# Kernel tuning notes

Measured on AMD Instinct MI355X. Metric: run time of the kernel, lower is better.

## Reference

```python
import jax, jax.numpy as jnp
import numpy as np

WEIGHT_FACTOR = 1.0
N_CLUSTERS = 64


def setup_inputs() -> dict:
    key = jax.random.key(0)
    k1, k2, k3 = jax.random.split(key, 3)
    B, H, W = 128, 256, 256
    x = jax.random.uniform(k1, (B, H, W), dtype=jnp.float32)
    pattern_importance = jax.random.uniform(k2, (B, N_CLUSTERS), dtype=jnp.float32)
    # dense cluster map: value in [0, N_CLUSTERS) = cluster id; == N_CLUSTERS = unassigned (mask stays 1)
    cluster_id = jax.random.randint(k3, (H, W), 0, N_CLUSTERS + 1, dtype=jnp.int32)
    return {"x": x, "pattern_importance": pattern_importance, "cluster_id": cluster_id}


def reference(x, pattern_importance, cluster_id):
    # FFT2 over last two dims; torch fftshift with dim=None shifts ALL axes (incl. batch),
    # and jnp.fft.fftshift has the same default semantics.
    x_fft = jnp.fft.fftshift(jnp.fft.fft2(x))
    assigned = cluster_id < N_CLUSTERS                     # [H, W] bool
    cid = jnp.where(assigned, cluster_id, 0)               # safe gather index
    vals = pattern_importance[:, cid] * WEIGHT_FACTOR      # [B, H, W] gather-built mask values
    mask = jnp.where(assigned[None, :, :], vals, jnp.float32(1.0))
    x_reject = x_fft * mask
    x_ifft = jnp.abs(jnp.fft.ifft2(jnp.fft.ifftshift(x_reject)))
    x_diff = jnp.abs(x_ifft - x)
    x_new = jnp.stack([x, x_ifft, x_diff], axis=1)         # [B, 3, H, W]
    return (x_new, pattern_importance)
```

## Files before the change

### kernel.cpp

```cpp
#include <hip/hip_runtime.h>
#include <hip/hip_fp16.h>
#include <math.h>

#define BB 128
#define HH 256
#define WW 256
#define HW 65536
#define OUT_B_STRIDE 196608

typedef float f32x4_t __attribute__((ext_vector_type(4)));

__device__ __forceinline__ void nt_store4(const float4 v, float4* p){
  f32x4_t t;
  t[0] = v.x; t[1] = v.y; t[2] = v.z; t[3] = v.w;
  __builtin_nontemporal_store(t, reinterpret_cast<f32x4_t*>(p));
}

__device__ __forceinline__ float2 cadd(float2 a, float2 b){ return make_float2(a.x+b.x, a.y+b.y); }
__device__ __forceinline__ float2 csub(float2 a, float2 b){ return make_float2(a.x-b.x, a.y-b.y); }

template<bool INV>
__device__ __forceinline__ float2 cmul_t(float2 a, float2 b){
  if (INV) return make_float2(a.x*b.x + a.y*b.y, a.y*b.x - a.x*b.y);
  return make_float2(a.x*b.x - a.y*b.y, a.x*b.y + a.y*b.x);
}

template<bool INV>
__device__ __forceinline__ void fft4(float2&a,float2&b,float2&c,float2&d){
  float2 t0 = cadd(a,c), t1 = csub(a,c);
  float2 t2 = cadd(b,d), t3 = csub(b,d);
  float2 t3r = INV ? make_float2(-t3.y, t3.x) : make_float2(t3.y, -t3.x);
  a = cadd(t0,t2);
  b = cadd(t1,t3r);
  c = csub(t0,t2);
  d = csub(t1,t3r);
}

template<bool INV>
__device__ __forceinline__ void fft16(float2 x[16]){
  #pragma unroll
  for (int j0=0;j0<4;++j0) fft4<INV>(x[j0], x[j0+4], x[j0+8], x[j0+12]);
  const float WR[10] = {1.f, 0.923879533f, 0.707106781f, 0.382683432f, 0.f,
                        0.f, -0.707106781f, 0.f, 0.f, -0.923879533f};
  const float WI[10] = {0.f, -0.382683432f, -0.707106781f, -0.923879533f, -1.f,
                        0.f, -0.707106781f, 0.f, 0.f, 0.382683432f};
  #pragma unroll
  for (int q0=1;q0<4;++q0)
    #pragma unroll
    for (int j0=1;j0<4;++j0){
      int k = j0*q0;
      x[j0+4*q0] = cmul_t<INV>(x[j0+4*q0], make_float2(WR[k], WI[k]));
    }
  #pragma unroll
  for (int q0=0;q0<4;++q0) fft4<INV>(x[4*q0], x[4*q0+1], x[4*q0+2], x[4*q0+3]);
  float2 t[16];
  #pragma unroll
  for (int q0=0;q0<4;++q0)
    #pragma unroll
    for (int q1=0;q1<4;++q1) t[q0+4*q1] = x[4*q0+q1];
  #pragma unroll
  for (int i=0;i<16;++i) x[i]=t[i];
}

__device__ __forceinline__ void build_tw256(float2* tw, int tid){
  float s,c;
  __sincosf(-6.28318530717958647692f * (float)tid / 256.0f, &s, &c);
  tw[tid] = make_float2(c, s);
}

__device__ __forceinline__ uint pkh2(float2 v){
  __half2 h = __float22half2_rn(v);
  return *(uint*)&h;
}
__device__ __forceinline__ float2 uph2(uint u){
  __half2 h = *(__half2*)&u;
  return __half22float2(h);
}

union SharedU {
  float  xs[16*272];
  float2 zbuf[16*273];
  float  ybuf[16*272];
};

__global__ __launch_bounds__(256, 4) void k_row_fwd(const float* __restrict__ x,
                                                    __half2* __restrict__ S,
                                                    const int* __restrict__ cid,
                                                    unsigned char* __restrict__ cidp){
  __shared__ SharedU sh;
  __shared__ float2 tw[256];
  int tid = threadIdx.x;
  int t = tid & 15, r = tid >> 4;
  build_tw256(tw, tid);

  if (blockIdx.x < 64){
    int g = (blockIdx.x*256 + tid) * 4;
    int p  = g >> 8;
    int s  = (g >> 4) & 15;
    int k1b = g & 15;
    int wfreq = 16*(p & 15) + (p >> 4);
    int w2 = (wfreq + 128) & 255;
    uchar4 v4;
    unsigned char* vp = (unsigned char*)&v4;
    #pragma unroll
    for (int i=0;i<4;++i){
      int h2 = (16*(k1b+i) + s + 128) & 255;
      int cv = cid[h2*256 + w2];
      vp[i] = (unsigned char)cv;
    }
    *(uchar4*)(cidp + g) = v4;
  }

  const float4* xb = (const float4*)x + (size_t)blockIdx.x * 1024;
  #pragma unroll
  for (int k=0;k<4;++k){
    int i2 = tid + k*256;
    float4 v = xb[i2];
    int row = i2 >> 6, c4 = i2 & 63;
    *(float4*)&sh.xs[row*272 + c4*4] = v;
  }
  __syncthreads();
  float2 X[16];
  #pragma unroll
  for (int j=0;j<16;++j) X[j] = make_float2(sh.xs[r*272 + 16*j + t], 0.f);
  __syncthreads();
  fft16<false>(X);
  #pragma unroll
  for (int q=0;q<16;++q) X[q] = cmul_t<false>(X[q], tw[t*q]);
  #pragma unroll
  for (int q=0;q<16;++q) sh.zbuf[r*273 + q*17 + t] = X[q];
  __syncthreads();
  float2 Y[16];
  #pragma unroll
  for (int tt=0;tt<16;++tt) Y[tt] = sh.zbuf[r*273 + t*17 + tt];
  fft16<false>(Y);
  int row = blockIdx.x*16 + r;
  int b = row >> 8, h = row & 255;
  uint4* dst = (uint4*)(S + (size_t)b*HW + h*256 + t*16);
  #pragma unroll
  for (int k=0;k<4;++k){
    uint4 q;
    q.x = pkh2(Y[4*k+0]); q.y = pkh2(Y[4*k+1]);
    q.z = pkh2(Y[4*k+2]); q.w = pkh2(Y[4*k+3]);
    dst[k] = q;
  }
}

__global__ __launch_bounds__(256, 4) void k_col(__half2* __restrict__ S,
                                                const unsigned char* __restrict__ cidp,
                                                const float* __restrict__ pi){
  __shared__ SharedU sh;
  __shared__ float2 tw[256];
  __shared__ float sPI[64];
  int tid = threadIdx.x;
  int c = tid & 15, t = tid >> 4;
  int cg = blockIdx.x, b = blockIdx.y;
  build_tw256(tw, tid);
  if (tid < 64) sPI[tid] = pi[(((b + 64) & 127) << 6) + tid] * 0.25f;
  __half2* Sb = S + (size_t)b*HW;
  int p = cg*16 + c;
  float2 X[16];
  #pragma unroll
  for (int j=0;j<16;++j) X[j] = uph2(*(uint*)&Sb[(16*j + t)*256 + p]);
  uint4 mq = *(const uint4*)(cidp + p*256 + t*16);
  __syncthreads();
  fft16<false>(X);
  #pragma unroll
  for (int q=0;q<16;++q) X[q] = cmul_t<false>(X[q], tw[t*q]);
  #pragma unroll
  for (int q=0;q<16;++q) sh.zbuf[c*273 + q*17 + t] = X[q];
  __syncthreads();
  int s = t;
  float2 Y[16];
  #pragma unroll
  for (int tt=0;tt<16;++tt) Y[tt] = sh.zbuf[c*273 + s*17 + tt];
  fft16<false>(Y);
  const uint* mw = (const uint*)&mq;
  #pragma unroll
  for (int k1=0;k1<16;++k1){
    int cv = (mw[k1>>2] >> ((k1&3)*8)) & 255;
    float m = (cv < 64) ? sPI[cv] : 0.25f;
    Y[k1].x *= m; Y[k1].y *= m;
  }
  __syncthreads();
  fft16<true>(Y);
  #pragma unroll
  for (int u=0;u<16;++u) Y[u] = cmul_t<true>(Y[u], tw[u*s]);
  #pragma unroll
  for (int u=0;u<16;++u) sh.zbuf[c*273 + u*17 + s] = Y[u];
  __syncthreads();
  float2 R[16];
  #pragma unroll
  for (int k0=0;k0<16;++k0) R[k0] = sh.zbuf[c*273 + t*17 + k0];
  fft16<true>(R);
  #pragma unroll
  for (int j=0;j<16;++j){
    uint u = pkh2(R[j]);
    *(uint*)&Sb[(16*j + t)*256 + p] = u;
  }
}

__global__ __launch_bounds__(256, 4) void k_row_inv_fused(const __half2* __restrict__ S,
                                                          const float* __restrict__ x,
                                                          const float* __restrict__ pi,
                                                          float* __restrict__ out){
  __shared__ SharedU sh;
  __shared__ float2 tw[256];
  int tid = threadIdx.x;
  int s = tid & 15, r = tid >> 4;
  int slice = blockIdx.x, b = blockIdx.y;
  build_tw256(tw, tid);
  int h = slice*16 + r;
  const uint4* src = (const uint4*)(S + (size_t)b*HW + h*256 + s*16);
  float2 X[16];
  #pragma unroll
  for (int k=0;k<4;++k){
    uint4 q = src[k];
    X[4*k+0] = uph2(q.x); X[4*k+1] = uph2(q.y);
    X[4*k+2] = uph2(q.z); X[4*k+3] = uph2(q.w);
  }
  __syncthreads();
  fft16<true>(X);
  #pragma unroll
  for (int u=0;u<16;++u) X[u] = cmul_t<true>(X[u], tw[u*s]);
  #pragma unroll
  for (int u=0;u<16;++u) sh.zbuf[r*273 + u*17 + s] = X[u];
  __syncthreads();
  float2 R[16];
  #pragma unroll
  for (int k0=0;k0<16;++k0) R[k0] = sh.zbuf[r*273 + s*17 + k0];
  fft16<true>(R);
  __syncthreads();
  const float scale = 1.0f/16384.0f;
  #pragma unroll
  for (int j=0;j<16;++j)
    sh.ybuf[r*272 + 16*j + s] = sqrtf(R[j].x*R[j].x + R[j].y*R[j].y) * scale;
  __syncthreads();
  const float4* x4 = (const float4*)x;
  float4* o4 = (float4*)out;
  size_t xbase = (size_t)b*16384 + slice*1024;
  size_t obase = (size_t)b*49152 + slice*1024;
  #pragma unroll
  for (int k=0;k<4;++k){
    int i2 = tid + k*256;
    int rr = i2 >> 6, c4 = i2 & 63;
    float4 y = *(float4*)&sh.ybuf[rr*272 + c4*4];
    float4 xv = x4[xbase + i2];
    float4 df;
    df.x = fabsf(y.x - xv.x); df.y = fabsf(y.y - xv.y);
    df.z = fabsf(y.z - xv.z); df.w = fabsf(y.w - xv.w);
    nt_store4(xv, &o4[obase + i2]);
    nt_store4(y,  &o4[obase + i2 + 16384]);
    nt_store4(df, &o4[obase + i2 + 32768]);
  }
  if (slice == 0 && b < 8){
    const float4* p4 = (const float4*)pi;
    nt_store4(p4[b*256 + tid], &o4[6291456 + b*256 + tid]);
  }
}

__global__ __launch_bounds__(256, 4) void k_row_inv_stage(const __half2* __restrict__ S,
                                                          float* __restrict__ out){
  __shared__ SharedU sh;
  __shared__ float2 tw[256];
  int tid = threadIdx.x;
  int s = tid & 15, r = tid >> 4;
  int slice = blockIdx.x, b = blockIdx.y;
  build_tw256(tw, tid);
  int h = slice*16 + r;
  const uint4* src = (const uint4*)(S + (size_t)b*HW + h*256 + s*16);
  float2 X[16];
  #pragma unroll
  for (int k=0;k<4;++k){
    uint4 q = src[k];
    X[4*k+0] = uph2(q.x); X[4*k+1] = uph2(q.y);
    X[4*k+2] = uph2(q.z); X[4*k+3] = uph2(q.w);
  }
  __syncthreads();
  fft16<true>(X);
  #pragma unroll
  for (int u=0;u<16;++u) X[u] = cmul_t<true>(X[u], tw[u*s]);
  #pragma unroll
  for (int u=0;u<16;++u) sh.zbuf[r*273 + u*17 + s] = X[u];
  __syncthreads();
  float2 R[16];
  #pragma unroll
  for (int k0=0;k0<16;++k0) R[k0] = sh.zbuf[r*273 + s*17 + k0];
  fft16<true>(R);
  const float scale = 1.0f/16384.0f;
  float* o = out + (size_t)b*OUT_B_STRIDE + h*256;
  #pragma unroll
  for (int j=0;j<16;++j)
    o[16*j + s] = sqrtf(R[j].x*R[j].x + R[j].y*R[j].y) * scale;
}

__global__ __launch_bounds__(256) void k_final(const float* __restrict__ x,
                                               const float* __restrict__ pi,
                                               float* __restrict__ out) {
  int i = blockIdx.x * 256 + threadIdx.x;
  const float4* x4 = (const float4*)x;
  float4* o4 = (float4*)out;
  int b = i >> 14;
  int r = i & 16383;
  int ch0 = b * 49152 + r;
  float4 y  = o4[ch0];
  float4 xv = x4[i];
  float4 df;
  df.x = fabsf(y.x - xv.x);
  df.y = fabsf(y.y - xv.y);
  df.z = fabsf(y.z - xv.z);
  df.w = fabsf(y.w - xv.w);
  nt_store4(xv, &o4[ch0]);
  nt_store4(y,  &o4[ch0 + 16384]);
  nt_store4(df, &o4[ch0 + 32768]);
  if (i < 2048) {
    const float4* p4 = (const float4*)pi;
    nt_store4(p4[i], &o4[6291456 + i]);
  }
}

extern "C" void kernel_launch(void* const* d_in, const int* in_sizes, int n_in,
                              void* d_out, int out_size, void* d_ws, size_t ws_size,
                              hipStream_t stream) {
  const float* x  = (const float*)d_in[0];
  const float* pi = (const float*)d_in[1];
  const int*  cid = (const int*)d_in[2];
  float* out = (float*)d_out;
  (void)in_sizes; (void)n_in; (void)out_size;

  const size_t S_bytes = (size_t)BB * HW * sizeof(__half2);
  const size_t cidp_bytes = 65536;

  if (ws_size >= S_bytes + cidp_bytes) {
    __half2* S = (__half2*)d_ws;
    unsigned char* cidp = (unsigned char*)d_ws + S_bytes;
    k_row_fwd<<<2048, 256, 0, stream>>>(x, S, cid, cidp);
    k_col<<<dim3(16, BB), 256, 0, stream>>>(S, cidp, pi);
    k_row_inv_fused<<<dim3(16, BB), 256, 0, stream>>>(S, x, pi, out);
  } else {
    __half2* S = (__half2*)out + (size_t)BB * HW;
    unsigned char* cidp = (unsigned char*)d_ws;
    k_row_fwd<<<2048, 256, 0, stream>>>(x, S, cid, cidp);
    k_col<<<dim3(16, BB), 256, 0, stream>>>(S, cidp, pi);
    k_row_inv_stage<<<dim3(16, BB), 256, 0, stream>>>(S, out);
    k_final<<<8192, 256, 0, stream>>>(x, pi, out);
  }
}
```

Baseline: 176.0 us.

## Replace block barriers with per-wavefront LDS regions and wave-local fences

Reorganizes thread-to-row mapping so each 64-lane wavefront owns a private LDS region and redundantly builds the full twiddle table. This lets most __syncthreads be replaced with a wave-local lgkmcnt wait, removing block-wide barrier stalls between FFT stages. The catch is that each wave now does four times the sincos work, and correctness depends on wavefront-synchronous execution and on the compiler honouring the inline asm as a memory fence. In k_col the column-to-lane mapping also changes, which alters global load coalescing.

New measurement: 179.6 us. 2.0% more time.

```diff
diff --git a/kernel.cpp b/kernel.cpp
--- a/kernel.cpp
+++ b/kernel.cpp
@@ -7,6 +7,8 @@
 #define WW 256
 #define HW 65536
 #define OUT_B_STRIDE 196608
+
+#define LDS_FENCE() asm volatile("s_waitcnt lgkmcnt(0)" ::: "memory")
 
 typedef float f32x4_t __attribute__((ext_vector_type(4)));
 
@@ -62,10 +64,14 @@
   for (int i=0;i<16;++i) x[i]=t[i];
 }
 
-__device__ __forceinline__ void build_tw256(float2* tw, int tid){
-  float s,c;
-  __sincosf(-6.28318530717958647692f * (float)tid / 256.0f, &s, &c);
-  tw[tid] = make_float2(c, s);
+__device__ __forceinline__ void build_tw_all(float2* tw, int lane){
+  #pragma unroll
+  for (int k=0;k<4;++k){
+    int idx = lane + 64*k;
+    float s,c;
+    __sincosf(-6.28318530717958647692f * (float)idx / 256.0f, &s, &c);
+    tw[idx] = make_float2(c, s);
+  }
 }
 
 __device__ __forceinline__ uint pkh2(float2 v){
@@ -83,15 +89,18 @@
   float  ybuf[16*272];
 };
 
+
 __global__ __launch_bounds__(256, 4) void k_row_fwd(const float* __restrict__ x,
                                                     __half2* __restrict__ S,
                                                     const int* __restrict__ cid,
                                                     unsigned char* __restrict__ cidp){
-  __shared__ SharedU sh;
+  __shared__ float2 zarena[4368];
   __shared__ float2 tw[256];
   int tid = threadIdx.x;
-  int t = tid & 15, r = tid >> 4;
-  build_tw256(tw, tid);
+  int lane = tid & 63, wid = tid >> 6;
+  int t = lane & 15, rl = lane >> 4;
+  int r = (wid << 2) + rl;
+  build_tw_all(tw, lane);
 
   if (blockIdx.x < 64){
     int g = (blockIdx.x*256 + tid) * 4;
@@ -112,27 +121,26 @@
   }
 
   const float4* xb = (const float4*)x + (size_t)blockIdx.x * 1024;
-  #pragma unroll
-  for (int k=0;k<4;++k){
-    int i2 = tid + k*256;
-    float4 v = xb[i2];
-    int row = i2 >> 6, c4 = i2 & 63;
-    *(float4*)&sh.xs[row*272 + c4*4] = v;
-  }
-  __syncthreads();
+  float* xsw = (float*)&zarena[wid*1092] + rl*272;
+  #pragma unroll
+  for (int j=0;j<4;++j){
+    float4 v = xb[r*64 + t + 16*j];
+    *(float4*)&xsw[4*(t + 16*j)] = v;
+  }
+  LDS_FENCE();
   float2 X[16];
   #pragma unroll
-  for (int j=0;j<16;++j) X[j] = make_float2(sh.xs[r*272 + 16*j + t], 0.f);
-  __syncthreads();
+  for (int j=0;j<16;++j) X[j] = make_float2(xsw[16*j + t], 0.f);
   fft16<false>(X);
   #pragma unroll
   for (int q=0;q<16;++q) X[q] = cmul_t<false>(X[q], tw[t*q]);
-  #pragma unroll
-  for (int q=0;q<16;++q) sh.zbuf[r*273 + q*17 + t] = X[q];
-  __syncthreads();
+  float2* zb = &zarena[wid*1092 + rl*273];
+  #pragma unroll
+  for (int q=0;q<16;++q) zb[q*17 + t] = X[q];
+  LDS_FENCE();
   float2 Y[16];
   #pragma unroll
-  for (int tt=0;tt<16;++tt) Y[tt] = sh.zbuf[r*273 + t*17 + tt];
+  for (int tt=0;tt<16;++tt) Y[tt] = zb[t*17 + tt];
   fft16<false>(Y);
   int row = blockIdx.x*16 + r;
   int b = row >> 8, h = row & 255;
@@ -149,31 +157,33 @@
 __global__ __launch_bounds__(256, 4) void k_col(__half2* __restrict__ S,
                                                 const unsigned char* __restrict__ cidp,
                                                 const float* __restrict__ pi){
-  __shared__ SharedU sh;
+  __shared__ float2 zarena[4368];
   __shared__ float2 tw[256];
   __shared__ float sPI[64];
   int tid = threadIdx.x;
-  int c = tid & 15, t = tid >> 4;
+  int lane = tid & 63, wid = tid >> 6;
+  int g = lane & 3, t = lane >> 2;
+  int c = (wid << 2) + g;
   int cg = blockIdx.x, b = blockIdx.y;
-  build_tw256(tw, tid);
-  if (tid < 64) sPI[tid] = pi[(((b + 64) & 127) << 6) + tid] * 0.25f;
+  build_tw_all(tw, lane);
+  sPI[lane] = pi[(((b + 64) & 127) << 6) + lane] * 0.25f;
   __half2* Sb = S + (size_t)b*HW;
   int p = cg*16 + c;
   float2 X[16];
   #pragma unroll
-  for (int j=0;j<16;++j) X[j] = uph2(*(uint*)&Sb[(16*j + t)*256 + p]);
+  for (int j=0;j<16;++j) X[j] = uph2(*(const uint*)&Sb[(16*j + t)*256 + p]);
   uint4 mq = *(const uint4*)(cidp + p*256 + t*16);
-  __syncthreads();
+  LDS_FENCE();
   fft16<false>(X);
   #pragma unroll
   for (int q=0;q<16;++q) X[q] = cmul_t<false>(X[q], tw[t*q]);
-  #pragma unroll
-  for (int q=0;q<16;++q) sh.zbuf[c*273 + q*17 + t] = X[q];
-  __syncthreads();
-  int s = t;
+  float2* zb = &zarena[c*273];
+  #pragma unroll
+  for (int q=0;q<16;++q) zb[q*17 + t] = X[q];
+  LDS_FENCE();
   float2 Y[16];
   #pragma unroll
-  for (int tt=0;tt<16;++tt) Y[tt] = sh.zbuf[c*273 + s*17 + tt];
+  for (int tt=0;tt<16;++tt) Y[tt] = zb[t*17 + tt];
   fft16<false>(Y);
   const uint* mw = (const uint*)&mq;
   #pragma unroll
@@ -182,21 +192,19 @@
     float m = (cv < 64) ? sPI[cv] : 0.25f;
     Y[k1].x *= m; Y[k1].y *= m;
   }
-  __syncthreads();
   fft16<true>(Y);
   #pragma unroll
-  for (int u=0;u<16;++u) Y[u] = cmul_t<true>(Y[u], tw[u*s]);
-  #pragma unroll
-  for (int u=0;u<16;++u) sh.zbuf[c*273 + u*17 + s] = Y[u];
-  __syncthreads();
+  for (int u=0;u<16;++u) Y[u] = cmul_t<true>(Y[u], tw[u*t]);
+  #pragma unroll
+  for (int u=0;u<16;++u) zb[u*17 + t] = Y[u];
+  LDS_FENCE();
   float2 R[16];
   #pragma unroll
-  for (int k0=0;k0<16;++k0) R[k0] = sh.zbuf[c*273 + t*17 + k0];
+  for (int k0=0;k0<16;++k0) R[k0] = zb[t*17 + k0];
   fft16<true>(R);
   #pragma unroll
   for (int j=0;j<16;++j){
-    uint u = pkh2(R[j]);
-    *(uint*)&Sb[(16*j + t)*256 + p] = u;
+    *(uint*)&Sb[(16*j + t)*256 + p] = pkh2(R[j]);
   }
 }
 
@@ -204,12 +212,14 @@
                                                           const float* __restrict__ x,
                                                           const float* __restrict__ pi,
                                                           float* __restrict__ out){
-  __shared__ SharedU sh;
+  __shared__ float2 zarena[4368];
   __shared__ float2 tw[256];
   int tid = threadIdx.x;
-  int s = tid & 15, r = tid >> 4;
+  int lane = tid & 63, wid = tid >> 6;
+  int s = lane & 15, rl = lane >> 4;
+  int r = (wid << 2) + rl;
   int slice = blockIdx.x, b = blockIdx.y;
-  build_tw256(tw, tid);
+  build_tw_all(tw, lane);
   int h = slice*16 + r;
   const uint4* src = (const uint4*)(S + (size_t)b*HW + h*256 + s*16);
   float2 X[16];
@@ -219,22 +229,23 @@
     X[4*k+0] = uph2(q.x); X[4*k+1] = uph2(q.y);
     X[4*k+2] = uph2(q.z); X[4*k+3] = uph2(q.w);
   }
-  __syncthreads();
+  LDS_FENCE();
   fft16<true>(X);
   #pragma unroll
   for (int u=0;u<16;++u) X[u] = cmul_t<true>(X[u], tw[u*s]);
-  #pragma unroll
-  for (int u=0;u<16;++u) sh.zbuf[r*273 + u*17 + s] = X[u];
-  __syncthreads();
+  float2* zb = &zarena[wid*1092 + rl*273];
+  #pragma unroll
+  for (int u=0;u<16;++u) zb[u*17 + s] = X[u];
+  LDS_FENCE();
   float2 R[16];
   #pragma unroll
-  for (int k0=0;k0<16;++k0) R[k0] = sh.zbuf[r*273 + s*17 + k0];
+  for (int k0=0;k0<16;++k0) R[k0] = zb[s*17 + k0];
   fft16<true>(R);
-  __syncthreads();
   const float scale = 1.0f/16384.0f;
+  float* yb = (float*)&zarena[wid*1092] + rl*272;
   #pragma unroll
   for (int j=0;j<16;++j)
-    sh.ybuf[r*272 + 16*j + s] = sqrtf(R[j].x*R[j].x + R[j].y*R[j].y) * scale;
+    yb[16*j + s] = sqrtf(R[j].x*R[j].x + R[j].y*R[j].y) * scale;
   __syncthreads();
   const float4* x4 = (const float4*)x;
   float4* o4 = (float4*)out;
@@ -244,7 +255,7 @@
   for (int k=0;k<4;++k){
     int i2 = tid + k*256;
     int rr = i2 >> 6, c4 = i2 & 63;
-    float4 y = *(float4*)&sh.ybuf[rr*272 + c4*4];
+    float4 y = *(float4*)((float*)&zarena[(rr>>2)*1092] + (rr&3)*272 + 4*c4);
     float4 xv = x4[xbase + i2];
     float4 df;
     df.x = fabsf(y.x - xv.x); df.y = fabsf(y.y - xv.y);
@@ -266,7 +277,7 @@
   int tid = threadIdx.x;
   int s = tid & 15, r = tid >> 4;
   int slice = blockIdx.x, b = blockIdx.y;
-  build_tw256(tw, tid);
+  build_tw_all(tw, tid & 63);
   int h = slice*16 + r;
   const uint4* src = (const uint4*)(S + (size_t)b*HW + h*256 + s*16);
   float2 X[16];
```

## Pack two real rows per complex FFT in forward row pass with wave-local LDS

Applied to the files above, without the earlier changes.

The forward row FFT now packs two real input rows into one complex FFT (even row as real part, odd as imaginary). It then separates the two spectra using conjugate symmetry, read back through LDS, which halves the forward-row FFT arithmetic and the grid size. Each wave owns a private LDS region and builds the full twiddle table itself, so s_waitcnt fences replace block-wide barriers. The cost is redundant twiddle sincos work (four per lane) in every kernel, an extra LDS round-trip for the split, and heavier register pressure.

Measured after the change: 179.2 us. Within noise of the previous version (+1.8%).

```diff
diff --git a/kernel.cpp b/kernel.cpp
--- a/kernel.cpp
+++ b/kernel.cpp
@@ -7,6 +7,8 @@
 #define WW 256
 #define HW 65536
 #define OUT_B_STRIDE 196608
+
+#define LDS_FENCE() asm volatile("s_waitcnt lgkmcnt(0)" ::: "memory")
 
 typedef float f32x4_t __attribute__((ext_vector_type(4)));
 
@@ -62,10 +64,14 @@
   for (int i=0;i<16;++i) x[i]=t[i];
 }
 
-__device__ __forceinline__ void build_tw256(float2* tw, int tid){
-  float s,c;
-  __sincosf(-6.28318530717958647692f * (float)tid / 256.0f, &s, &c);
-  tw[tid] = make_float2(c, s);
+__device__ __forceinline__ void build_tw_all(float2* tw, int lane){
+  #pragma unroll
+  for (int k=0;k<4;++k){
+    int idx = lane + 64*k;
+    float s,c;
+    __sincosf(-6.28318530717958647692f * (float)idx / 256.0f, &s, &c);
+    tw[idx] = make_float2(c, s);
+  }
 }
 
 __device__ __forceinline__ uint pkh2(float2 v){
@@ -87,11 +93,12 @@
                                                     __half2* __restrict__ S,
                                                     const int* __restrict__ cid,
                                                     unsigned char* __restrict__ cidp){
-  __shared__ SharedU sh;
+  __shared__ float2 zarena[4368];
   __shared__ float2 tw[256];
   int tid = threadIdx.x;
-  int t = tid & 15, r = tid >> 4;
-  build_tw256(tw, tid);
+  int lane = tid & 63, wid = tid >> 6;
+  int t = lane & 15, rl = lane >> 4;
+  build_tw_all(tw, lane);
 
   if (blockIdx.x < 64){
     int g = (blockIdx.x*256 + tid) * 4;
@@ -111,38 +118,57 @@
     *(uchar4*)(cidp + g) = v4;
   }
 
-  const float4* xb = (const float4*)x + (size_t)blockIdx.x * 1024;
-  #pragma unroll
-  for (int k=0;k<4;++k){
-    int i2 = tid + k*256;
-    float4 v = xb[i2];
-    int row = i2 >> 6, c4 = i2 & 63;
-    *(float4*)&sh.xs[row*272 + c4*4] = v;
-  }
-  __syncthreads();
-  float2 X[16];
-  #pragma unroll
-  for (int j=0;j<16;++j) X[j] = make_float2(sh.xs[r*272 + 16*j + t], 0.f);
-  __syncthreads();
-  fft16<false>(X);
-  #pragma unroll
-  for (int q=0;q<16;++q) X[q] = cmul_t<false>(X[q], tw[t*q]);
-  #pragma unroll
-  for (int q=0;q<16;++q) sh.zbuf[r*273 + q*17 + t] = X[q];
-  __syncthreads();
+  const float4* xb = (const float4*)x + (size_t)blockIdx.x * 2048;
+  float* xsw = (float*)&zarena[wid*1092];
+  #pragma unroll
+  for (int j=0;j<8;++j){
+    float4 v = xb[(wid*8 + j)*64 + lane];
+    *(float4*)&xsw[j*272 + lane*4] = v;
+  }
+  LDS_FENCE();
+
+  float2 Z[16];
+  #pragma unroll
+  for (int j=0;j<16;++j)
+    Z[j] = make_float2(xsw[(2*rl)*272 + 16*j + t],
+                       xsw[(2*rl+1)*272 + 16*j + t]);
+  fft16<false>(Z);
+  #pragma unroll
+  for (int q=0;q<16;++q) Z[q] = cmul_t<false>(Z[q], tw[t*q]);
+  float2* zb = &zarena[wid*1092 + rl*273];
+  #pragma unroll
+  for (int q=0;q<16;++q) zb[q*17 + t] = Z[q];
+  LDS_FENCE();
   float2 Y[16];
   #pragma unroll
-  for (int tt=0;tt<16;++tt) Y[tt] = sh.zbuf[r*273 + t*17 + tt];
+  for (int tt=0;tt<16;++tt) Y[tt] = zb[t*17 + tt];
   fft16<false>(Y);
-  int row = blockIdx.x*16 + r;
-  int b = row >> 8, h = row & 255;
-  uint4* dst = (uint4*)(S + (size_t)b*HW + h*256 + t*16);
-  #pragma unroll
-  for (int k=0;k<4;++k){
-    uint4 q;
-    q.x = pkh2(Y[4*k+0]); q.y = pkh2(Y[4*k+1]);
-    q.z = pkh2(Y[4*k+2]); q.w = pkh2(Y[4*k+3]);
-    dst[k] = q;
+
+  #pragma unroll
+  for (int k1=0;k1<16;++k1) zb[k1*17 + t] = Y[k1];
+  LDS_FENCE();
+  int sel = (t == 0) ? 1 : 0;
+  int tp = (16 - t) & 15;
+  uint qE[16], qO[16];
+  #pragma unroll
+  for (int k1=0;k1<16;++k1){
+    float2 M = zb[((15 - k1 + sel) & 15)*17 + tp];
+    float2 Ze = make_float2(0.5f*(Y[k1].x + M.x), 0.5f*(Y[k1].y - M.y));
+    float2 Zo = make_float2(0.5f*(Y[k1].y + M.y), 0.5f*(M.x - Y[k1].x));
+    qE[k1] = pkh2(Ze);
+    qO[k1] = pkh2(Zo);
+  }
+
+  int row0 = blockIdx.x*32 + (wid<<3) + 2*rl;
+  int b = row0 >> 8, h = row0 & 255;
+  uint4* dstE = (uint4*)(S + (size_t)b*HW + h*256 + t*16);
+  uint4* dstO = (uint4*)(S + (size_t)b*HW + (h+1)*256 + t*16);
+  #pragma unroll
+  for (int k=0;k<4;++k){
+    uint4 qe; qe.x = qE[4*k+0]; qe.y = qE[4*k+1]; qe.z = qE[4*k+2]; qe.w = qE[4*k+3];
+    uint4 qo; qo.x = qO[4*k+0]; qo.y = qO[4*k+1]; qo.z = qO[4*k+2]; qo.w = qO[4*k+3];
+    dstE[k] = qe;
+    dstO[k] = qo;
   }
 }
 
@@ -155,13 +181,13 @@
   int tid = threadIdx.x;
   int c = tid & 15, t = tid >> 4;
   int cg = blockIdx.x, b = blockIdx.y;
-  build_tw256(tw, tid);
+  build_tw_all(tw, tid & 63);
   if (tid < 64) sPI[tid] = pi[(((b + 64) & 127) << 6) + tid] * 0.25f;
   __half2* Sb = S + (size_t)b*HW;
   int p = cg*16 + c;
   float2 X[16];
   #pragma unroll
-  for (int j=0;j<16;++j) X[j] = uph2(*(uint*)&Sb[(16*j + t)*256 + p]);
+  for (int j=0;j<16;++j) X[j] = uph2(*(const uint*)&Sb[(16*j + t)*256 + p]);
   uint4 mq = *(const uint4*)(cidp + p*256 + t*16);
   __syncthreads();
   fft16<false>(X);
@@ -195,8 +221,7 @@
   fft16<true>(R);
   #pragma unroll
   for (int j=0;j<16;++j){
-    uint u = pkh2(R[j]);
-    *(uint*)&Sb[(16*j + t)*256 + p] = u;
+    *(uint*)&Sb[(16*j + t)*256 + p] = pkh2(R[j]);
   }
 }
 
@@ -209,7 +234,7 @@
   int tid = threadIdx.x;
   int s = tid & 15, r = tid >> 4;
   int slice = blockIdx.x, b = blockIdx.y;
-  build_tw256(tw, tid);
+  build_tw_all(tw, tid & 63);
   int h = slice*16 + r;
   const uint4* src = (const uint4*)(S + (size_t)b*HW + h*256 + s*16);
   float2 X[16];
@@ -266,7 +291,7 @@
   int tid = threadIdx.x;
   int s = tid & 15, r = tid >> 4;
   int slice = blockIdx.x, b = blockIdx.y;
-  build_tw256(tw, tid);
+  build_tw_all(tw, tid & 63);
   int h = slice*16 + r;
   const uint4* src = (const uint4*)(S + (size_t)b*HW + h*256 + s*16);
   float2 X[16];
@@ -334,13 +359,13 @@
   if (ws_size >= S_bytes + cidp_bytes) {
     __half2* S = (__half2*)d_ws;
     unsigned char* cidp = (unsigned char*)d_ws + S_bytes;
-    k_row_fwd<<<2048, 256, 0, stream>>>(x, S, cid, cidp);
+    k_row_fwd<<<1024, 256, 0, stream>>>(x, S, cid, cidp);
     k_col<<<dim3(16, BB), 256, 0, stream>>>(S, cidp, pi);
     k_row_inv_fused<<<dim3(16, BB), 256, 0, stream>>>(S, x, pi, out);
   } else {
     __half2* S = (__half2*)out + (size_t)BB * HW;
     unsigned char* cidp = (unsigned char*)d_ws;
-    k_row_fwd<<<2048, 256, 0, stream>>>(x, S, cid, cidp);
+    k_row_fwd<<<1024, 256, 0, stream>>>(x, S, cid, cidp);
     k_col<<<dim3(16, BB), 256, 0, stream>>>(S, cidp, pi);
     k_row_inv_stage<<<dim3(16, BB), 256, 0, stream>>>(S, out);
     k_final<<<8192, 256, 0, stream>>>(x, pi, out);
```
